# Kernel optimization log

Hardware: AMD Instinct MI355X
Metric: run time of the kernel (lower is better)

The kernel has to match this reference:

```python
import jax, jax.numpy as jnp
import numpy as np

MLOG32 = float(np.log(32.0))


def _maxpool(x, k):
    # F.max_pool2d(stride=1, padding=k//2) pads with -inf, matching init value
    pad = k // 2
    return jax.lax.reduce_window(x, -jnp.inf, jax.lax.max, (1, 1, k, k), (1, 1, 1, 1),
                                 ((0, 0), (0, 0), (pad, pad), (pad, pad)))


def _minpool(x, k):
    return -_maxpool(-x, k)


def _local_sum(x, k):
    # conv2d with all-ones kxk kernel, zero padding, same spatial size
    pad = k // 2
    return jax.lax.reduce_window(x, 0.0, jax.lax.add, (1, 1, k, k), (1, 1, 1, 1),
                                 ((0, 0), (0, 0), (pad, pad), (pad, pad)))


def _conv3(x, kern):
    # torch conv2d == cross-correlation == lax conv (no kernel flip)
    return jax.lax.conv_general_dilated(x, kern, (1, 1), ((1, 1), (1, 1)),
                                        dimension_numbers=('NCHW', 'OIHW', 'NCHW'))


def _otsu(gray, bins=32):
    # vectorized per-batch Otsu threshold; gray in [0,1]
    B, _, H, W = gray.shape
    v = gray.reshape(B, -1)
    idx = jnp.clip((v * bins).astype(jnp.int32), 0, bins - 1)  # histc semantics, v==1 -> last bin
    hist = jax.vmap(lambda i: jnp.bincount(i, length=bins))(idx).astype(gray.dtype)
    p = hist / (H * W + 1e-6)
    xs = jnp.linspace(0.0, 1.0, bins, dtype=gray.dtype)
    omega = jnp.cumsum(p, axis=1)
    mu = jnp.cumsum(p * xs[None, :], axis=1)
    mu_t = mu[:, -1:]
    sigma_b2 = (mu_t * omega - mu) ** 2 / (omega * (1.0 - omega) + 1e-8)
    kbest = jnp.argmax(sigma_b2, axis=1)
    edges = jnp.linspace(0.0, 1.0, bins + 1, dtype=gray.dtype)
    return edges[kbest].reshape(B, 1, 1, 1)


def _concept_maps(image_rgb, cell_dilate=10, k_local=9):
    r, g, b = image_rgb[:, 0:1], image_rgb[:, 1:2], image_rgb[:, 2:3]
    gray = jnp.clip(0.5 * (0.299 * r + 0.587 * g + 0.114 * b + 1.0), 0.0, 1.0)
    thr = _otsu(gray)
    nuc = (gray <= thr).astype(gray.dtype)
    # morphological open+close, k=3
    e = _minpool(nuc, 3)
    d = _maxpool(e, 3)
    d = _maxpool(d, 3)
    e2 = _minpool(d, 3)
    nuc = (e2 > 0.5).astype(gray.dtype)
    er = _minpool(nuc, 3)
    boundary = jnp.maximum(nuc - er, 0.0)
    lap_k = jnp.array([[0, 1, 0], [1, -4, 1], [0, 1, 0]], dtype=gray.dtype).reshape(1, 1, 3, 3)
    lap = jnp.abs(_conv3(nuc, lap_k))
    den = _local_sum(boundary, 5) + 1e-6
    roughness = lap * boundary / den
    kx = jnp.array([[1, 0, -1], [2, 0, -2], [1, 0, -1]], dtype=gray.dtype).reshape(1, 1, 3, 3)
    ky = jnp.array([[1, 2, 1], [0, 0, 0], [-1, -2, -1]], dtype=gray.dtype).reshape(1, 1, 3, 3)
    gx = _conv3(gray, kx)
    gy = _conv3(gray, ky)
    ang = jnp.arctan2(gy, gx)
    den_orient = _local_sum(jnp.ones_like(gray), k_local) + 1e-6
    ms = _local_sum(jnp.sin(ang), k_local) / den_orient
    mc = _local_sum(jnp.cos(ang), k_local) / den_orient
    circ_var = 1.0 - jnp.sqrt(ms ** 2 + mc ** 2 + 1e-6)
    kd = cell_dilate if cell_dilate % 2 == 1 else cell_dilate + 1  # force odd
    cell = jnp.minimum(_maxpool(nuc, kd), 1.0)
    A_n = _local_sum(nuc, k_local)
    A_c = jnp.maximum(_local_sum(cell, k_local) - A_n, 1.0)
    nc = A_n / A_c
    g2 = _local_sum(gray * gray, k_local) / den_orient
    g1 = _local_sum(gray, k_local) / den_orient
    ent_like = jnp.log1p(jnp.maximum(g2 - g1 * g1, 0.0))
    z_maps = jnp.concatenate([roughness, circ_var, nc, ent_like], axis=1)
    return z_maps, nuc


def _energy_forward(image_rgb, cal_a, cal_b, alpha_logits, tau_p, Ht, Wt):
    z_maps, nuc = _concept_maps(image_rgb)
    z0 = jnp.log1p(jnp.maximum(z_maps[:, 0:1], 0.0))
    z1 = jnp.clip(z_maps[:, 1:2], 0.0, 1.0)
    z2 = jnp.log1p(jnp.maximum(z_maps[:, 2:3], 0.0))
    z3 = jnp.clip(z_maps[:, 3:4], 0.0, MLOG32)
    z_stable = jnp.concatenate([z0, z1, z2, z3], axis=1)
    z_cal = jax.nn.softplus(cal_a)[None, :, None, None] * z_stable + cal_b[None, :, None, None]
    alpha = jax.nn.softmax(alpha_logits)[None, :, None, None]
    E = jnp.sum(alpha * z_cal, axis=1, keepdims=True)
    B = E.shape[0]
    if (E.shape[2], E.shape[3]) != (Ht, Wt):
        E_t = jax.image.resize(E, (B, 1, Ht, Wt), method='linear')
    else:
        E_t = E
    tau = 0.2 + jax.nn.softplus(tau_p)
    A = jax.nn.softmax((-E_t / tau).reshape(B, 1, Ht * Wt), axis=-1).reshape(B, 1, Ht, Wt)
    return A, z_maps, nuc, E_t


def setup_inputs() -> dict:
    key = jax.random.key(0)
    k1, k2, k3, k4 = jax.random.split(key, 4)
    B, H, W = 16, 512, 512
    image_rgb = 2.0 * jax.random.uniform(k1, (B, 3, H, W), dtype=jnp.float32) - 1.0
    cal_a = 1.0 + 0.1 * jax.random.normal(k2, (4,), jnp.float32)
    cal_b = 0.1 * jax.random.normal(k3, (4,), jnp.float32)
    alpha_logits = 0.1 * jax.random.normal(k4, (4,), jnp.float32)
    tau_p = jnp.float32(0.5)
    return {"image_rgb": image_rgb, "cal_a": cal_a, "cal_b": cal_b,
            "alpha_logits": alpha_logits, "tau_p": tau_p, "target_h": 512, "target_w": 512}


def reference(image_rgb, cal_a, cal_b, alpha_logits, tau_p, target_h, target_w):
    return _energy_forward(image_rgb, cal_a, cal_b, alpha_logits, tau_p, int(target_h), int(target_w))
```

## Files before the change

kernel.cpp:

```cpp
#include <hip/hip_runtime.h>
#include <math.h>
#include <stdint.h>

#define HW 512
#define IMG (HW*HW)
#define MLOG32f 3.4657359027997265f

__device__ __forceinline__ float grayf(float r, float g, float b) {
    float t = __fadd_rn(__fadd_rn(__fmul_rn(0.299f, r), __fmul_rn(0.587f, g)), __fmul_rn(0.114f, b));
    float s = __fmul_rn(0.5f, __fadd_rn(t, 1.0f));
    return fminf(fmaxf(s, 0.0f), 1.0f);
}

__device__ __forceinline__ float softplusf(float x) {
    return fmaxf(x, 0.0f) + log1pf(expf(-fabsf(x)));
}

__device__ __forceinline__ float frcp(float x)  { return __builtin_amdgcn_rcpf(x); }
__device__ __forceinline__ float frsq(float x)  { return __builtin_amdgcn_rsqf(x); }
__device__ __forceinline__ float flog1p(float x){ return __logf(1.0f + x); }

__device__ __forceinline__ uint64_t kmask(int lo, int hi) {
    return (1ull << hi) - (1ull << lo);
}

__global__ void k_init(const float* __restrict__ cal_a, const float* __restrict__ cal_b,
                       const float* __restrict__ alpha_logits, const float* __restrict__ tau_p,
                       int* __restrict__ hist, float* __restrict__ expsum,
                       float* __restrict__ sc, int B) {
    int tid = threadIdx.x;
    for (int i = tid; i < B * 32; i += blockDim.x) hist[i] = 0;
    for (int i = tid; i < B; i += blockDim.x) expsum[i] = 0.0f;
    if (tid == 0) {
        float al[4];
        float m = -1e30f;
        for (int c = 0; c < 4; c++) { al[c] = alpha_logits[c]; m = fmaxf(m, al[c]); }
        float e[4]; float s = 0.0f;
        for (int c = 0; c < 4; c++) { e[c] = expf(al[c] - m); s += e[c]; }
        float bias = 0.0f;
        for (int c = 0; c < 4; c++) {
            float alpha = e[c] / s;
            sc[c] = alpha * softplusf(cal_a[c]);
            bias += alpha * cal_b[c];
        }
        sc[4] = bias;
        float tau = 0.2f + softplusf(tau_p[0]);
        sc[5] = tau;
        sc[6] = -1.0f / tau;
    }
}

__global__ __launch_bounds__(256) void k_gray_hist(const float* __restrict__ img,
                                                   float* __restrict__ gray,
                                                   int* __restrict__ hist) {
    __shared__ int lh[32];
    int tid = threadIdx.x;
    int b = blockIdx.y;
    if (tid < 32) lh[tid] = 0;
    __syncthreads();
    const float4* rp = (const float4*)(img + (size_t)b * 3 * IMG);
    const float4* gp = (const float4*)(img + (size_t)b * 3 * IMG + IMG);
    const float4* bp = (const float4*)(img + (size_t)b * 3 * IMG + 2 * IMG);
    float4* op = (float4*)(gray + (size_t)b * IMG);
    int i = blockIdx.x * 256 + tid;
    float4 r = rp[i], g = gp[i], bb = bp[i];
    float4 o;
    o.x = grayf(r.x, g.x, bb.x);
    o.y = grayf(r.y, g.y, bb.y);
    o.z = grayf(r.z, g.z, bb.z);
    o.w = grayf(r.w, g.w, bb.w);
    op[i] = o;
    int b0 = min(max((int)(o.x * 32.0f), 0), 31);
    int b1 = min(max((int)(o.y * 32.0f), 0), 31);
    int b2 = min(max((int)(o.z * 32.0f), 0), 31);
    int b3 = min(max((int)(o.w * 32.0f), 0), 31);
    atomicAdd(&lh[b0], 1); atomicAdd(&lh[b1], 1);
    atomicAdd(&lh[b2], 1); atomicAdd(&lh[b3], 1);
    __syncthreads();
    if (tid < 32) atomicAdd(&hist[b * 32 + tid], lh[tid]);
}

__global__ void k_otsu(const int* __restrict__ hist, float* __restrict__ thr, int B) {
    int b = threadIdx.x;
    if (b >= B) return;
    const int* h = hist + b * 32;
    float omega[32], mu[32];
    float co = 0.0f, cm = 0.0f;
    for (int k = 0; k < 32; k++) {
        float pk = (float)h[k] * (1.0f / 262144.0f);
        float xs = (float)((double)k / 31.0);
        co += pk;
        cm += pk * xs;
        omega[k] = co; mu[k] = cm;
    }
    float mu_t = mu[31];
    float best = -1e30f; int kb = 0;
    for (int k = 0; k < 32; k++) {
        float t = mu_t * omega[k] - mu[k];
        float sb = (t * t) / (omega[k] * (1.0f - omega[k]) + 1e-8f);
        if (sb > best) { best = sb; kb = k; }
    }
    thr[b] = (float)kb * 0.03125f;
}

__global__ __launch_bounds__(256) void k_thresh(const float* __restrict__ gray,
                                                const float* __restrict__ thr,
                                                uint32_t* __restrict__ packed) {
    int b = blockIdx.y;
    int i = blockIdx.x * 256 + threadIdx.x;
    float t = thr[b];
    float v = gray[(size_t)b * IMG + i];
    unsigned long long m = __ballot(v <= t);
    if ((threadIdx.x & 63) == 0)
        *(uint64_t*)&packed[(size_t)b * 8192 + (i >> 5)] = m;
}

__global__ __launch_bounds__(256) void k_morph(const uint32_t* __restrict__ p0,
                                               uint32_t* __restrict__ pn) {
    __shared__ uint64_t s0[40], s1[40];
    int tid = threadIdx.x, b = blockIdx.z;
    int x0 = blockIdx.x * 32, y0 = blockIdx.y * 32;
    int w0 = x0 >> 5;
    const uint32_t* pb = p0 + (size_t)b * 8192;
    int xlo = (x0 == 0) ? 4 : 0;
    int xhi = (x0 == 480) ? 36 : 40;
    uint64_t mwin = kmask(xlo, xhi);

    if (tid < 40) {
        int y = y0 - 4 + tid;
        uint64_t v = 0;
        if ((unsigned)y < (unsigned)HW) {
            const uint32_t* rowp = pb + y * 16;
            uint64_t wm = (w0 > 0)  ? rowp[w0 - 1] : 0;
            uint64_t wc = rowp[w0];
            uint64_t wp = (w0 < 15) ? rowp[w0 + 1] : 0;
            v = ((wm >> 28) | (wc << 4) | (wp << 36)) & kmask(0, 40);
        }
        s0[tid] = v;
    }
    __syncthreads();
    if (tid >= 1 && tid < 39) {
        uint64_t e = ~0ull;
        for (int dq = -1; dq <= 1; dq++) {
            int q = tid + dq;
            int y = y0 - 4 + q;
            uint64_t m = ((unsigned)y < (unsigned)HW) ? mwin : 0;
            uint64_t v = s0[q] | ~m;
            e &= v & (v << 1) & (v >> 1);
        }
        s1[tid] = e;
    }
    __syncthreads();
    if (tid >= 2 && tid < 38) {
        uint64_t d = 0;
        uint64_t me = kmask(1, 39);
        for (int dq = -1; dq <= 1; dq++) {
            int q = tid + dq;
            int y = y0 - 4 + q;
            uint64_t m = ((unsigned)y < (unsigned)HW) ? (mwin & me) : 0;
            uint64_t v = s1[q] & m;
            d |= v | (v << 1) | (v >> 1);
        }
        s0[tid] = d;
    }
    __syncthreads();
    if (tid >= 3 && tid < 37) {
        uint64_t d = 0;
        uint64_t me = kmask(2, 38);
        for (int dq = -1; dq <= 1; dq++) {
            int q = tid + dq;
            int y = y0 - 4 + q;
            uint64_t m = ((unsigned)y < (unsigned)HW) ? (mwin & me) : 0;
            uint64_t v = s0[q] & m;
            d |= v | (v << 1) | (v >> 1);
        }
        s1[tid] = d;
    }
    __syncthreads();
    if (tid >= 4 && tid < 36) {
        uint64_t e = ~0ull;
        uint64_t me = kmask(3, 37);
        for (int dq = -1; dq <= 1; dq++) {
            int q = tid + dq;
            int y = y0 - 4 + q;
            uint64_t m = ((unsigned)y < (unsigned)HW) ? (mwin & me) : 0;
            uint64_t v = s1[q] | ~m;
            e &= v & (v << 1) & (v >> 1);
        }
        s0[tid] = e;
    }
    __syncthreads();
    if (tid < 32) {
        int y = y0 + tid;
        pn[(size_t)b * 8192 + y * 16 + w0] = (uint32_t)(s0[tid + 4] >> 4);
    }
}

__global__ __launch_bounds__(256) void k_maps(const float* __restrict__ gray,
                                              const uint32_t* __restrict__ pn,
                                              float* __restrict__ zmap,
                                              float* __restrict__ nucf,
                                              float* __restrict__ Eout,
                                              const float* __restrict__ sc,
                                              float* __restrict__ expsum) {
    __shared__ __align__(16) char smem[30912];
    __shared__ uint64_t nrow[50], ehr[50], dilh[50], bnd[36], cell[40];
    __shared__ float red[4];
    float* gt  = (float*)smem;
    float* st  = (float*)(smem + 7232);
    float* ct  = (float*)(smem + 13792);
    float* rs0 = (float*)(smem + 20352);
    float* rs1 = (float*)(smem + 25632);
    int* rs_n = (int*)smem;
    int* rs_c = (int*)(smem + 5120);
    int* rs_b = (int*)(smem + 10240);

    int tid = threadIdx.x, b = blockIdx.z;
    int x0 = blockIdx.x * 32, y0 = blockIdx.y * 32;
    int w0 = x0 >> 5;
    const float* gb = gray + (size_t)b * IMG;
    const uint32_t* pb = pn + (size_t)b * 8192;
    int xlo = (x0 == 0) ? 9 : 0;
    int xhi = (x0 == 480) ? 41 : 50;
    uint64_t mwin = kmask(xlo, xhi);

    for (int i = tid; i < 42 * 42; i += 256) {
        int ly = i / 42, lx = i % 42;
        int gy = y0 + ly - 5, gx = x0 + lx - 5;
        gt[ly * 43 + lx] = (gy >= 0 && gy < HW && gx >= 0 && gx < HW) ? gb[gy * HW + gx] : 0.0f;
    }
    if (tid < 50) {
        int y = y0 - 9 + tid;
        uint64_t v = 0;
        if ((unsigned)y < (unsigned)HW) {
            const uint32_t* rowp = pb + y * 16;
            uint64_t wm = (w0 > 0)  ? rowp[w0 - 1] : 0;
            uint64_t wc = rowp[w0];
            uint64_t wp = (w0 < 15) ? rowp[w0 + 1] : 0;
            v = ((wm >> 23) | (wc << 9) | (wp << 41)) & kmask(0, 50);
        }
        nrow[tid] = v;
    }
    __syncthreads();

    if (tid < 50) {
        uint64_t v = nrow[tid];
        uint64_t d = v | (v << 1) | (v >> 1);
        d = d | (d << 2) | (d >> 2);
        d = d | (d << 2) | (d >> 2);
        dilh[tid] = d;
    }
    if (tid >= 6 && tid < 44) {
        int y = y0 - 9 + tid;
        uint64_t m = ((unsigned)y < (unsigned)HW) ? mwin : 0;
        uint64_t v = nrow[tid] | ~m;
        ehr[tid] = v & (v << 1) & (v >> 1);
    }
    for (int i = tid; i < 1600; i += 256) {
        int ly = i / 40, lx = i % 40;
        int gy = y0 + ly - 4, gx = x0 + lx - 4;
        float s = 0.0f, c = 0.0f;
        if (gy >= 0 && gy < HW && gx >= 0 && gx < HW) {
            float a00 = gt[ly * 43 + lx],       a01 = gt[ly * 43 + lx + 1],       a02 = gt[ly * 43 + lx + 2];
            float a10 = gt[(ly + 1) * 43 + lx],                                   a12 = gt[(ly + 1) * 43 + lx + 2];
            float a20 = gt[(ly + 2) * 43 + lx], a21 = gt[(ly + 2) * 43 + lx + 1], a22 = gt[(ly + 2) * 43 + lx + 2];
            float gxv = (a00 - a02) + 2.0f * (a10 - a12) + (a20 - a22);
            float gyv = (a00 + 2.0f * a01 + a02) - (a20 + 2.0f * a21 + a22);
            float r2 = gxv * gxv + gyv * gyv;
            if (r2 > 0.0f) { float ir = frsq(r2); s = gyv * ir; c = gxv * ir; }
            else { s = 0.0f; c = 1.0f; }
        }
        st[ly * 41 + lx] = s; ct[ly * 41 + lx] = c;
    }
    __syncthreads();

    if (tid < 36) {
        int r = tid + 7;
        uint64_t er = ehr[r - 1] & ehr[r] & ehr[r + 1];
        bnd[tid] = nrow[r] & ~er;
    }
    if (tid < 40) {
        int r = tid + 5;
        int y = y0 - 4 + tid;
        uint64_t c = 0;
        for (int d = -5; d <= 5; d++) c |= dilh[r + d];
        uint64_t m = ((unsigned)y < (unsigned)HW) ? mwin : 0;
        cell[tid] = c & m;
    }
    for (int i = tid; i < 40 * 32; i += 256) {
        int ly = i >> 5, lx = i & 31;
        float ss = 0.0f, cs = 0.0f;
        for (int dx = 0; dx < 9; dx++) { ss += st[ly * 41 + lx + dx]; cs += ct[ly * 41 + lx + dx]; }
        rs0[ly * 33 + lx] = ss; rs1[ly * 33 + lx] = cs;
    }
    __syncthreads();

    float z1v[4];
    for (int k = 0; k < 4; k++) {
        int j = tid + k * 256; int py = j >> 5, px = j & 31;
        float ss = 0.0f, cs = 0.0f;
        for (int dy = 0; dy < 9; dy++) { ss += rs0[(py + dy) * 33 + px]; cs += rs1[(py + dy) * 33 + px]; }
        int gy = y0 + py, gx = x0 + px;
        float cnty = (float)(min(gy + 4, HW - 1) - max(gy - 4, 0) + 1);
        float cntx = (float)(min(gx + 4, HW - 1) - max(gx - 4, 0) + 1);
        float iden = frcp(cnty * cntx + 1e-6f);
        float ms = ss * iden, mc = cs * iden;
        z1v[k] = 1.0f - sqrtf(ms * ms + mc * mc + 1e-6f);
    }
    __syncthreads();
    for (int i = tid; i < 40 * 32; i += 256) {
        int ly = i >> 5, lx = i & 31;
        float gs = 0.0f, g2s = 0.0f;
        for (int dx = 1; dx <= 9; dx++) { float v = gt[(ly + 1) * 43 + lx + dx]; gs += v; g2s += v * v; }
        rs0[ly * 33 + lx] = gs; rs1[ly * 33 + lx] = g2s;
    }
    __syncthreads();
    float z3v[4];
    for (int k = 0; k < 4; k++) {
        int j = tid + k * 256; int py = j >> 5, px = j & 31;
        float gs = 0.0f, g2s = 0.0f;
        for (int dy = 0; dy < 9; dy++) { gs += rs0[(py + dy) * 33 + px]; g2s += rs1[(py + dy) * 33 + px]; }
        int gy = y0 + py, gx = x0 + px;
        float cnty = (float)(min(gy + 4, HW - 1) - max(gy - 4, 0) + 1);
        float cntx = (float)(min(gx + 4, HW - 1) - max(gx - 4, 0) + 1);
        float iden = frcp(cnty * cntx + 1e-6f);
        float g1 = gs * iden, g2 = g2s * iden;
        z3v[k] = flog1p(fmaxf(g2 - g1 * g1, 0.0f));
    }
    __syncthreads();

    for (int i = tid; i < 40 * 32; i += 256) {
        int rr = i >> 5, p = i & 31;
        rs_n[rr * 32 + p] = __popcll((nrow[rr + 5] >> (p + 5)) & 0x1FFull);
        rs_c[rr * 32 + p] = __popcll((cell[rr]     >> (p + 5)) & 0x1FFull);
    }
    for (int i = tid; i < 36 * 32; i += 256) {
        int rr = i >> 5, p = i & 31;
        rs_b[rr * 32 + p] = __popcll((bnd[rr] >> (p + 7)) & 0x1Full);
    }
    __syncthreads();
    if (tid < 96) {
        int p = tid & 31, a = tid >> 5;
        if (a == 0)      { int s = 0; for (int rr = 0; rr < 40; rr++) { s += rs_n[rr * 32 + p]; rs_n[rr * 32 + p] = s; } }
        else if (a == 1) { int s = 0; for (int rr = 0; rr < 40; rr++) { s += rs_c[rr * 32 + p]; rs_c[rr * 32 + p] = s; } }
        else             { int s = 0; for (int rr = 0; rr < 36; rr++) { s += rs_b[rr * 32 + p]; rs_b[rr * 32 + p] = s; } }
    }
    __syncthreads();

    float w0f = sc[0], w1f = sc[1], w2f = sc[2], w3f = sc[3], bias = sc[4], ntau = sc[6];
    float* z0p = zmap + ((size_t)b * 4 + 0) * IMG;
    float* z1p = zmap + ((size_t)b * 4 + 1) * IMG;
    float* z2p = zmap + ((size_t)b * 4 + 2) * IMG;
    float* z3p = zmap + ((size_t)b * 4 + 3) * IMG;
    float* Ep  = Eout + (size_t)b * IMG;
    float* np  = nucf + (size_t)b * IMG;
    float acc = 0.0f;
    for (int k = 0; k < 4; k++) {
        int j = tid + k * 256; int py = j >> 5, p = j & 31;
        int An = rs_n[(py + 8) * 32 + p] - (py ? rs_n[(py - 1) * 32 + p] : 0);
        int Ac = rs_c[(py + 8) * 32 + p] - (py ? rs_c[(py - 1) * 32 + p] : 0);
        int db = rs_b[(py + 4) * 32 + p] - (py ? rs_b[(py - 1) * 32 + p] : 0);
        int r = py + 9, kk = p + 9;
        uint64_t rowc = nrow[r];
        int cbit = (int)((rowc >> kk) & 1);
        int nb4  = (int)((nrow[r - 1] >> kk) & 1) + (int)((nrow[r + 1] >> kk) & 1)
                 + (int)((rowc >> (kk - 1)) & 1) + (int)((rowc >> (kk + 1)) & 1);
        int lap = nb4 - 4 * cbit; lap = lap < 0 ? -lap : lap;
        int bc  = (int)((bnd[py + 2] >> kk) & 1);
        float rough = (float)(lap * bc) * frcp((float)db + 1e-6f);
        float z2 = (float)An * frcp(fmaxf((float)(Ac - An), 1.0f));
        float z0s = flog1p(fmaxf(rough, 0.0f));
        float z1s = fminf(fmaxf(z1v[k], 0.0f), 1.0f);
        float z2s = flog1p(fmaxf(z2, 0.0f));
        float z3s = fminf(fmaxf(z3v[k], 0.0f), MLOG32f);
        float E = w0f * z0s + w1f * z1s + w2f * z2s + w3f * z3s + bias;
        int gy = y0 + py, gx = x0 + p;
        size_t o = (size_t)gy * HW + gx;
        z0p[o] = rough;
        z1p[o] = z1v[k];
        z2p[o] = z2;
        z3p[o] = z3v[k];
        Ep[o]  = E;
        np[o]  = (float)cbit;
        acc += __expf(E * ntau);
    }
    for (int off = 32; off > 0; off >>= 1) acc += __shfl_down(acc, off, 64);
    if ((tid & 63) == 0) red[tid >> 6] = acc;
    __syncthreads();
    if (tid == 0) atomicAdd(&expsum[b], red[0] + red[1] + red[2] + red[3]);
}

__global__ __launch_bounds__(256) void k_softmaxA(const float* __restrict__ E,
                                                  float* __restrict__ A,
                                                  const float* __restrict__ sc,
                                                  const float* __restrict__ expsum) {
    int b = blockIdx.y;
    int i = blockIdx.x * 256 + threadIdx.x;
    float ntau = sc[6];
    float invS = 1.0f / expsum[b];
    const float4* Ep = (const float4*)(E + (size_t)b * IMG);
    float4* Ap = (float4*)(A + (size_t)b * IMG);
    float4 e = Ep[i];
    float4 o;
    o.x = __expf(e.x * ntau) * invS;
    o.y = __expf(e.y * ntau) * invS;
    o.z = __expf(e.z * ntau) * invS;
    o.w = __expf(e.w * ntau) * invS;
    Ap[i] = o;
}

extern "C" void kernel_launch(void* const* d_in, const int* in_sizes, int n_in,
                              void* d_out, int out_size, void* d_ws, size_t ws_size,
                              hipStream_t stream) {
    const float* img   = (const float*)d_in[0];
    const float* cal_a = (const float*)d_in[1];
    const float* cal_b = (const float*)d_in[2];
    const float* alpha = (const float*)d_in[3];
    const float* tau_p = (const float*)d_in[4];
    int B = in_sizes[0] / (3 * IMG);

    float* out  = (float*)d_out;
    float* A    = out;
    float* zmap = out + (size_t)B * IMG;
    float* nuc  = out + (size_t)B * IMG * 5;
    float* E    = out + (size_t)B * IMG * 6;
    float* gray = A;

    int*      hist    = (int*)d_ws;
    float*    thr     = (float*)d_ws + B * 32;
    float*    sc      = thr + B;
    float*    expsum  = sc + 8;
    uint32_t* packed0 = (uint32_t*)d_ws + 1024;
    uint32_t* packedN = packed0 + (size_t)B * 8192;

    k_init<<<1, 256, 0, stream>>>(cal_a, cal_b, alpha, tau_p, hist, expsum, sc, B);
    k_gray_hist<<<dim3(IMG / 1024, B), 256, 0, stream>>>(img, gray, hist);
    k_otsu<<<1, 64, 0, stream>>>(hist, thr, B);
    k_thresh<<<dim3(IMG / 256, B), 256, 0, stream>>>(gray, thr, packed0);
    dim3 tg(HW / 32, HW / 32, B);
    k_morph<<<tg, 256, 0, stream>>>(packed0, packedN);
    k_maps<<<tg, 256, 0, stream>>>(gray, packedN, zmap, nuc, E, sc, expsum);
    k_softmaxA<<<dim3(IMG / 1024, B), 256, 0, stream>>>(E, A, sc, expsum);
}
```

Before: 257.5 us.

## Use sliding-window box sums, ballot-based histogram, and merge init into Otsu kernel

Replaces the per-pixel 9-tap horizontal and vertical box sums in k_maps with sliding-window sums, where each thread computes 4 adjacent outputs incrementally. It also drops the serial column prefix-scan pass for the popcount-based counts. The shared-memory histogram atomics become wave ballots over bit planes plus popcount, with one atomic per bin per wave. The separate init kernel is replaced by a memset, and the scalar-parameter computation moves into the Otsu kernel, saving a launch. Sliding sums change the float summation order slightly, and the wave ballot assumes 64-lane wavefronts.

```diff
diff --git a/kernel.cpp b/kernel.cpp
--- a/kernel.cpp
+++ b/kernel.cpp
@@ -22,32 +22,6 @@
 
 __device__ __forceinline__ uint64_t kmask(int lo, int hi) {
     return (1ull << hi) - (1ull << lo);
-}
-
-__global__ void k_init(const float* __restrict__ cal_a, const float* __restrict__ cal_b,
-                       const float* __restrict__ alpha_logits, const float* __restrict__ tau_p,
-                       int* __restrict__ hist, float* __restrict__ expsum,
-                       float* __restrict__ sc, int B) {
-    int tid = threadIdx.x;
-    for (int i = tid; i < B * 32; i += blockDim.x) hist[i] = 0;
-    for (int i = tid; i < B; i += blockDim.x) expsum[i] = 0.0f;
-    if (tid == 0) {
-        float al[4];
-        float m = -1e30f;
-        for (int c = 0; c < 4; c++) { al[c] = alpha_logits[c]; m = fmaxf(m, al[c]); }
-        float e[4]; float s = 0.0f;
-        for (int c = 0; c < 4; c++) { e[c] = expf(al[c] - m); s += e[c]; }
-        float bias = 0.0f;
-        for (int c = 0; c < 4; c++) {
-            float alpha = e[c] / s;
-            sc[c] = alpha * softplusf(cal_a[c]);
-            bias += alpha * cal_b[c];
-        }
-        sc[4] = bias;
-        float tau = 0.2f + softplusf(tau_p[0]);
-        sc[5] = tau;
-        sc[6] = -1.0f / tau;
-    }
 }
 
 __global__ __launch_bounds__(256) void k_gray_hist(const float* __restrict__ img,
@@ -70,37 +44,76 @@
     o.z = grayf(r.z, g.z, bb.z);
     o.w = grayf(r.w, g.w, bb.w);
     op[i] = o;
-    int b0 = min(max((int)(o.x * 32.0f), 0), 31);
-    int b1 = min(max((int)(o.y * 32.0f), 0), 31);
-    int b2 = min(max((int)(o.z * 32.0f), 0), 31);
-    int b3 = min(max((int)(o.w * 32.0f), 0), 31);
-    atomicAdd(&lh[b0], 1); atomicAdd(&lh[b1], 1);
-    atomicAdd(&lh[b2], 1); atomicAdd(&lh[b3], 1);
+    int idx[4];
+    idx[0] = min(max((int)(o.x * 32.0f), 0), 31);
+    idx[1] = min(max((int)(o.y * 32.0f), 0), 31);
+    idx[2] = min(max((int)(o.z * 32.0f), 0), 31);
+    idx[3] = min(max((int)(o.w * 32.0f), 0), 31);
+    int lane = tid & 63;
+    int bin = lane & 31;
+    int cnt = 0;
+    #pragma unroll
+    for (int e = 0; e < 4; e++) {
+        int v = idx[e];
+        unsigned long long m0 = __ballot((v & 1)  != 0);
+        unsigned long long m1 = __ballot((v & 2)  != 0);
+        unsigned long long m2 = __ballot((v & 4)  != 0);
+        unsigned long long m3 = __ballot((v & 8)  != 0);
+        unsigned long long m4 = __ballot((v & 16) != 0);
+        unsigned long long mm = (bin & 1)  ? m0 : ~m0;
+        mm &= (bin & 2)  ? m1 : ~m1;
+        mm &= (bin & 4)  ? m2 : ~m2;
+        mm &= (bin & 8)  ? m3 : ~m3;
+        mm &= (bin & 16) ? m4 : ~m4;
+        cnt += __popcll(mm);
+    }
+    if (lane < 32) atomicAdd(&lh[bin], cnt);
     __syncthreads();
     if (tid < 32) atomicAdd(&hist[b * 32 + tid], lh[tid]);
 }
 
-__global__ void k_otsu(const int* __restrict__ hist, float* __restrict__ thr, int B) {
-    int b = threadIdx.x;
-    if (b >= B) return;
-    const int* h = hist + b * 32;
-    float omega[32], mu[32];
-    float co = 0.0f, cm = 0.0f;
-    for (int k = 0; k < 32; k++) {
-        float pk = (float)h[k] * (1.0f / 262144.0f);
-        float xs = (float)((double)k / 31.0);
-        co += pk;
-        cm += pk * xs;
-        omega[k] = co; mu[k] = cm;
-    }
-    float mu_t = mu[31];
-    float best = -1e30f; int kb = 0;
-    for (int k = 0; k < 32; k++) {
-        float t = mu_t * omega[k] - mu[k];
-        float sb = (t * t) / (omega[k] * (1.0f - omega[k]) + 1e-8f);
-        if (sb > best) { best = sb; kb = k; }
-    }
-    thr[b] = (float)kb * 0.03125f;
+__global__ void k_otsu_sc(const int* __restrict__ hist,
+                          const float* __restrict__ cal_a, const float* __restrict__ cal_b,
+                          const float* __restrict__ alpha_logits, const float* __restrict__ tau_p,
+                          float* __restrict__ thr, float* __restrict__ sc, int B) {
+    int tid = threadIdx.x;
+    if (tid < B) {
+        const int* h = hist + tid * 32;
+        float omega[32], mu[32];
+        float co = 0.0f, cm = 0.0f;
+        for (int k = 0; k < 32; k++) {
+            float pk = (float)h[k] * (1.0f / 262144.0f);
+            float xs = (float)((double)k / 31.0);
+            co += pk;
+            cm += pk * xs;
+            omega[k] = co; mu[k] = cm;
+        }
+        float mu_t = mu[31];
+        float best = -1e30f; int kb = 0;
+        for (int k = 0; k < 32; k++) {
+            float t = mu_t * omega[k] - mu[k];
+            float sb = (t * t) / (omega[k] * (1.0f - omega[k]) + 1e-8f);
+            if (sb > best) { best = sb; kb = k; }
+        }
+        thr[tid] = (float)kb * 0.03125f;
+    }
+    if (tid == 63) {
+        float al[4];
+        float m = -1e30f;
+        for (int c = 0; c < 4; c++) { al[c] = alpha_logits[c]; m = fmaxf(m, al[c]); }
+        float e[4]; float s = 0.0f;
+        for (int c = 0; c < 4; c++) { e[c] = expf(al[c] - m); s += e[c]; }
+        float bias = 0.0f;
+        for (int c = 0; c < 4; c++) {
+            float alpha = e[c] / s;
+            sc[c] = alpha * softplusf(cal_a[c]);
+            bias += alpha * cal_b[c];
+        }
+        sc[4] = bias;
+        float tau = 0.2f + softplusf(tau_p[0]);
+        sc[5] = tau;
+        sc[6] = -1.0f / tau;
+    }
 }
 
 __global__ __launch_bounds__(256) void k_thresh(const float* __restrict__ gray,
@@ -205,7 +218,6 @@
                                               float* __restrict__ expsum) {
     __shared__ __align__(16) char smem[30912];
     __shared__ uint64_t nrow[50], ehr[50], dilh[50], bnd[36], cell[40];
-    __shared__ float red[4];
     float* gt  = (float*)smem;
     float* st  = (float*)(smem + 7232);
     float* ct  = (float*)(smem + 13792);
@@ -214,6 +226,7 @@
     int* rs_n = (int*)smem;
     int* rs_c = (int*)(smem + 5120);
     int* rs_b = (int*)(smem + 10240);
+    float* red = (float*)(smem + 16384);
 
     int tid = threadIdx.x, b = blockIdx.z;
     int x0 = blockIdx.x * 32, y0 = blockIdx.y * 32;
@@ -287,63 +300,92 @@
         uint64_t m = ((unsigned)y < (unsigned)HW) ? mwin : 0;
         cell[tid] = c & m;
     }
+    for (int i = tid; i < 320; i += 256) {
+        int ly = i >> 3, c0 = (i & 7) << 2;
+        int base = ly * 41 + c0;
+        float sa[12], ca[12];
+        #pragma unroll
+        for (int j = 0; j < 12; j++) { sa[j] = st[base + j]; ca[j] = ct[base + j]; }
+        float ss = sa[0]+sa[1]+sa[2]+sa[3]+sa[4]+sa[5]+sa[6]+sa[7]+sa[8];
+        float cs = ca[0]+ca[1]+ca[2]+ca[3]+ca[4]+ca[5]+ca[6]+ca[7]+ca[8];
+        int ob = ly * 33 + c0;
+        rs0[ob] = ss; rs1[ob] = cs;
+        #pragma unroll
+        for (int q = 1; q < 4; q++) {
+            ss += sa[8 + q] - sa[q - 1];
+            cs += ca[8 + q] - ca[q - 1];
+            rs0[ob + q] = ss; rs1[ob + q] = cs;
+        }
+    }
+    __syncthreads();
+
+    int p = tid & 31, py0 = (tid >> 5) << 2;
+    int gx = x0 + p;
+    float cntx = (float)(min(gx + 4, HW - 1) - max(gx - 4, 0) + 1);
+    float z1v[4], z3v[4];
+    {
+        float s[12], c[12];
+        #pragma unroll
+        for (int j = 0; j < 12; j++) { s[j] = rs0[(py0 + j) * 33 + p]; c[j] = rs1[(py0 + j) * 33 + p]; }
+        float ss = s[0]+s[1]+s[2]+s[3]+s[4]+s[5]+s[6]+s[7]+s[8];
+        float cs = c[0]+c[1]+c[2]+c[3]+c[4]+c[5]+c[6]+c[7]+c[8];
+        #pragma unroll
+        for (int q = 0; q < 4; q++) {
+            int gy = y0 + py0 + q;
+            float cnty = (float)(min(gy + 4, HW - 1) - max(gy - 4, 0) + 1);
+            float iden = frcp(cnty * cntx + 1e-6f);
+            float ms = ss * iden, mc = cs * iden;
+            z1v[q] = 1.0f - sqrtf(ms * ms + mc * mc + 1e-6f);
+            if (q < 3) { ss += s[9 + q] - s[q]; cs += c[9 + q] - c[q]; }
+        }
+    }
+    __syncthreads();
+
+    for (int i = tid; i < 320; i += 256) {
+        int ly = i >> 3, c0 = (i & 7) << 2;
+        int base = (ly + 1) * 43 + c0 + 1;
+        float v[12];
+        #pragma unroll
+        for (int j = 0; j < 12; j++) v[j] = gt[base + j];
+        float gs = v[0]+v[1]+v[2]+v[3]+v[4]+v[5]+v[6]+v[7]+v[8];
+        float g2 = v[0]*v[0]+v[1]*v[1]+v[2]*v[2]+v[3]*v[3]+v[4]*v[4]+v[5]*v[5]+v[6]*v[6]+v[7]*v[7]+v[8]*v[8];
+        int ob = ly * 33 + c0;
+        rs0[ob] = gs; rs1[ob] = g2;
+        #pragma unroll
+        for (int q = 1; q < 4; q++) {
+            gs += v[8 + q] - v[q - 1];
+            g2 += v[8 + q] * v[8 + q] - v[q - 1] * v[q - 1];
+            rs0[ob + q] = gs; rs1[ob + q] = g2;
+        }
+    }
+    __syncthreads();
+
+    {
+        float s[12], c[12];
+        #pragma unroll
+        for (int j = 0; j < 12; j++) { s[j] = rs0[(py0 + j) * 33 + p]; c[j] = rs1[(py0 + j) * 33 + p]; }
+        float gs = s[0]+s[1]+s[2]+s[3]+s[4]+s[5]+s[6]+s[7]+s[8];
+        float g2 = c[0]+c[1]+c[2]+c[3]+c[4]+c[5]+c[6]+c[7]+c[8];
+        #pragma unroll
+        for (int q = 0; q < 4; q++) {
+            int gy = y0 + py0 + q;
+            float cnty = (float)(min(gy + 4, HW - 1) - max(gy - 4, 0) + 1);
+            float iden = frcp(cnty * cntx + 1e-6f);
+            float g1 = gs * iden, gq = g2 * iden;
+            z3v[q] = flog1p(fmaxf(gq - g1 * g1, 0.0f));
+            if (q < 3) { gs += s[9 + q] - s[q]; g2 += c[9 + q] - c[q]; }
+        }
+    }
+    __syncthreads();
+
     for (int i = tid; i < 40 * 32; i += 256) {
-        int ly = i >> 5, lx = i & 31;
-        float ss = 0.0f, cs = 0.0f;
-        for (int dx = 0; dx < 9; dx++) { ss += st[ly * 41 + lx + dx]; cs += ct[ly * 41 + lx + dx]; }
-        rs0[ly * 33 + lx] = ss; rs1[ly * 33 + lx] = cs;
-    }
-    __syncthreads();
-
-    float z1v[4];
-    for (int k = 0; k < 4; k++) {
-        int j = tid + k * 256; int py = j >> 5, px = j & 31;
-        float ss = 0.0f, cs = 0.0f;
-        for (int dy = 0; dy < 9; dy++) { ss += rs0[(py + dy) * 33 + px]; cs += rs1[(py + dy) * 33 + px]; }
-        int gy = y0 + py, gx = x0 + px;
-        float cnty = (float)(min(gy + 4, HW - 1) - max(gy - 4, 0) + 1);
-        float cntx = (float)(min(gx + 4, HW - 1) - max(gx - 4, 0) + 1);
-        float iden = frcp(cnty * cntx + 1e-6f);
-        float ms = ss * iden, mc = cs * iden;
-        z1v[k] = 1.0f - sqrtf(ms * ms + mc * mc + 1e-6f);
-    }
-    __syncthreads();
-    for (int i = tid; i < 40 * 32; i += 256) {
-        int ly = i >> 5, lx = i & 31;
-        float gs = 0.0f, g2s = 0.0f;
-        for (int dx = 1; dx <= 9; dx++) { float v = gt[(ly + 1) * 43 + lx + dx]; gs += v; g2s += v * v; }
-        rs0[ly * 33 + lx] = gs; rs1[ly * 33 + lx] = g2s;
-    }
-    __syncthreads();
-    float z3v[4];
-    for (int k = 0; k < 4; k++) {
-        int j = tid + k * 256; int py = j >> 5, px = j & 31;
-        float gs = 0.0f, g2s = 0.0f;
-        for (int dy = 0; dy < 9; dy++) { gs += rs0[(py + dy) * 33 + px]; g2s += rs1[(py + dy) * 33 + px]; }
-        int gy = y0 + py, gx = x0 + px;
-        float cnty = (float)(min(gy + 4, HW - 1) - max(gy - 4, 0) + 1);
-        float cntx = (float)(min(gx + 4, HW - 1) - max(gx - 4, 0) + 1);
-        float iden = frcp(cnty * cntx + 1e-6f);
-        float g1 = gs * iden, g2 = g2s * iden;
-        z3v[k] = flog1p(fmaxf(g2 - g1 * g1, 0.0f));
-    }
-    __syncthreads();
-
-    for (int i = tid; i < 40 * 32; i += 256) {
-        int rr = i >> 5, p = i & 31;
-        rs_n[rr * 32 + p] = __popcll((nrow[rr + 5] >> (p + 5)) & 0x1FFull);
-        rs_c[rr * 32 + p] = __popcll((cell[rr]     >> (p + 5)) & 0x1FFull);
+        int rr = i >> 5, pp = i & 31;
+        rs_n[rr * 32 + pp] = __popcll((nrow[rr + 5] >> (pp + 5)) & 0x1FFull);
+        rs_c[rr * 32 + pp] = __popcll((cell[rr]     >> (pp + 5)) & 0x1FFull);
     }
     for (int i = tid; i < 36 * 32; i += 256) {
-        int rr = i >> 5, p = i & 31;
-        rs_b[rr * 32 + p] = __popcll((bnd[rr] >> (p + 7)) & 0x1Full);
-    }
-    __syncthreads();
-    if (tid < 96) {
-        int p = tid & 31, a = tid >> 5;
-        if (a == 0)      { int s = 0; for (int rr = 0; rr < 40; rr++) { s += rs_n[rr * 32 + p]; rs_n[rr * 32 + p] = s; } }
-        else if (a == 1) { int s = 0; for (int rr = 0; rr < 40; rr++) { s += rs_c[rr * 32 + p]; rs_c[rr * 32 + p] = s; } }
-        else             { int s = 0; for (int rr = 0; rr < 36; rr++) { s += rs_b[rr * 32 + p]; rs_b[rr * 32 + p] = s; } }
+        int rr = i >> 5, pp = i & 31;
+        rs_b[rr * 32 + pp] = __popcll((bnd[rr] >> (pp + 7)) & 0x1Full);
     }
     __syncthreads();
 
@@ -355,34 +397,48 @@
     float* Ep  = Eout + (size_t)b * IMG;
     float* np  = nucf + (size_t)b * IMG;
     float acc = 0.0f;
-    for (int k = 0; k < 4; k++) {
-        int j = tid + k * 256; int py = j >> 5, p = j & 31;
-        int An = rs_n[(py + 8) * 32 + p] - (py ? rs_n[(py - 1) * 32 + p] : 0);
-        int Ac = rs_c[(py + 8) * 32 + p] - (py ? rs_c[(py - 1) * 32 + p] : 0);
-        int db = rs_b[(py + 4) * 32 + p] - (py ? rs_b[(py - 1) * 32 + p] : 0);
-        int r = py + 9, kk = p + 9;
-        uint64_t rowc = nrow[r];
-        int cbit = (int)((rowc >> kk) & 1);
-        int nb4  = (int)((nrow[r - 1] >> kk) & 1) + (int)((nrow[r + 1] >> kk) & 1)
-                 + (int)((rowc >> (kk - 1)) & 1) + (int)((rowc >> (kk + 1)) & 1);
-        int lap = nb4 - 4 * cbit; lap = lap < 0 ? -lap : lap;
-        int bc  = (int)((bnd[py + 2] >> kk) & 1);
-        float rough = (float)(lap * bc) * frcp((float)db + 1e-6f);
-        float z2 = (float)An * frcp(fmaxf((float)(Ac - An), 1.0f));
-        float z0s = flog1p(fmaxf(rough, 0.0f));
-        float z1s = fminf(fmaxf(z1v[k], 0.0f), 1.0f);
-        float z2s = flog1p(fmaxf(z2, 0.0f));
-        float z3s = fminf(fmaxf(z3v[k], 0.0f), MLOG32f);
-        float E = w0f * z0s + w1f * z1s + w2f * z2s + w3f * z3s + bias;
-        int gy = y0 + py, gx = x0 + p;
-        size_t o = (size_t)gy * HW + gx;
-        z0p[o] = rough;
-        z1p[o] = z1v[k];
-        z2p[o] = z2;
-        z3p[o] = z3v[k];
-        Ep[o]  = E;
-        np[o]  = (float)cbit;
-        acc += __expf(E * ntau);
+    {
+        int nn[12], cc[12], bb8[8];
+        #pragma unroll
+        for (int j = 0; j < 12; j++) { nn[j] = rs_n[(py0 + j) * 32 + p]; cc[j] = rs_c[(py0 + j) * 32 + p]; }
+        #pragma unroll
+        for (int j = 0; j < 8; j++) bb8[j] = rs_b[(py0 + j) * 32 + p];
+        int An = nn[0]+nn[1]+nn[2]+nn[3]+nn[4]+nn[5]+nn[6]+nn[7]+nn[8];
+        int Ac = cc[0]+cc[1]+cc[2]+cc[3]+cc[4]+cc[5]+cc[6]+cc[7]+cc[8];
+        int db = bb8[0]+bb8[1]+bb8[2]+bb8[3]+bb8[4];
+        int kk = p + 9;
+        #pragma unroll
+        for (int q = 0; q < 4; q++) {
+            int py = py0 + q;
+            int r = py + 9;
+            uint64_t rowc = nrow[r];
+            int cbit = (int)((rowc >> kk) & 1);
+            int nb4  = (int)((nrow[r - 1] >> kk) & 1) + (int)((nrow[r + 1] >> kk) & 1)
+                     + (int)((rowc >> (kk - 1)) & 1) + (int)((rowc >> (kk + 1)) & 1);
+            int lap = nb4 - 4 * cbit; lap = lap < 0 ? -lap : lap;
+            int bc  = (int)((bnd[py + 2] >> kk) & 1);
+            float rough = (float)(lap * bc) * frcp((float)db + 1e-6f);
+            float z2 = (float)An * frcp(fmaxf((float)(Ac - An), 1.0f));
+            float z0s = flog1p(fmaxf(rough, 0.0f));
+            float z1s = fminf(fmaxf(z1v[q], 0.0f), 1.0f);
+            float z2s = flog1p(fmaxf(z2, 0.0f));
+            float z3s = fminf(fmaxf(z3v[q], 0.0f), MLOG32f);
+            float E = w0f * z0s + w1f * z1s + w2f * z2s + w3f * z3s + bias;
+            int gy = y0 + py;
+            size_t o = (size_t)gy * HW + x0 + p;
+            z0p[o] = rough;
+            z1p[o] = z1v[q];
+            z2p[o] = z2;
+            z3p[o] = z3v[q];
+            Ep[o]  = E;
+            np[o]  = (float)cbit;
+            acc += __expf(E * ntau);
+            if (q < 3) {
+                An += nn[9 + q] - nn[q];
+                Ac += cc[9 + q] - cc[q];
+                db += bb8[5 + q] - bb8[q];
+            }
+        }
     }
     for (int off = 32; off > 0; off >>= 1) acc += __shfl_down(acc, off, 64);
     if ((tid & 63) == 0) red[tid >> 6] = acc;
@@ -427,15 +483,15 @@
     float* gray = A;
 
     int*      hist    = (int*)d_ws;
-    float*    thr     = (float*)d_ws + B * 32;
+    float*    expsum  = (float*)d_ws + B * 32;
+    float*    thr     = expsum + B;
     float*    sc      = thr + B;
-    float*    expsum  = sc + 8;
     uint32_t* packed0 = (uint32_t*)d_ws + 1024;
     uint32_t* packedN = packed0 + (size_t)B * 8192;
 
-    k_init<<<1, 256, 0, stream>>>(cal_a, cal_b, alpha, tau_p, hist, expsum, sc, B);
+    hipMemsetAsync(d_ws, 0, (size_t)(B * 32 + B) * 4, stream);
     k_gray_hist<<<dim3(IMG / 1024, B), 256, 0, stream>>>(img, gray, hist);
-    k_otsu<<<1, 64, 0, stream>>>(hist, thr, B);
+    k_otsu_sc<<<1, 64, 0, stream>>>(hist, cal_a, cal_b, alpha, tau_p, thr, sc, B);
     k_thresh<<<dim3(IMG / 256, B), 256, 0, stream>>>(gray, thr, packed0);
     dim3 tg(HW / 32, HW / 32, B);
     k_morph<<<tg, 256, 0, stream>>>(packed0, packedN);
```

After: 247.8 us. 1.04x faster.
